# Performance work log

Measured on AMD Instinct MI355X. Metric: run time of the kernel, lower is better.

## Reference

```python
import jax, jax.numpy as jnp
import numpy as np

NH = 8          # n_heads
EPS = 1e-12     # layer_norm_eps


def _ln(x, g, b, eps=EPS):
    m = x.mean(-1, keepdims=True)
    v = jnp.var(x, axis=-1, keepdims=True)
    return (x - m) / jnp.sqrt(v + eps) * g + b


def _heads(x):
    # [B,S,H] -> [B,NH,S,H/NH]
    B, S, H = x.shape
    return x.reshape(B, S, NH, H // NH).transpose(0, 2, 1, 3)


def setup_inputs() -> dict:
    B, S, H, INNER = 32, 512, 512, 2048
    n_items = 50000
    std = 0.02
    ks = list(jax.random.split(jax.random.key(0), 20))
    inp = {}
    inp['x'] = jax.random.normal(ks[0], (B, S, H), jnp.float32)
    inp['value_input'] = jax.random.normal(ks[1], (B, S, H), jnp.float32)
    inp['beha_emb'] = jax.random.normal(ks[2], (B, S, H), jnp.float32)
    inp['pos_table'] = std * jax.random.normal(ks[3], (S, H), jnp.float32)
    names = ['q', 'k', 'v', 'pk', 'pq', 'bk', 'bq', 'd']
    for i, n in enumerate(names):
        inp['W' + n] = std * jax.random.normal(ks[4 + i], (H, H), jnp.float32)
        inp['b' + n] = jnp.zeros((H,), jnp.float32)
    inp['ln_g'] = jnp.ones((H,), jnp.float32)
    inp['ln_b'] = jnp.zeros((H,), jnp.float32)
    inp['W1'] = std * jax.random.normal(ks[12], (H, INNER), jnp.float32)
    inp['b1'] = jnp.zeros((INNER,), jnp.float32)
    inp['W2'] = std * jax.random.normal(ks[13], (INNER, H), jnp.float32)
    inp['b2'] = jnp.zeros((H,), jnp.float32)
    inp['ln2_g'] = jnp.ones((H,), jnp.float32)
    inp['ln2_b'] = jnp.zeros((H,), jnp.float32)
    inp['item_seq'] = jax.random.randint(ks[14], (B, S), 0, n_items, jnp.int32)
    return inp


def reference(x, value_input, beha_emb, pos_table, Wq, bq, Wk, bk, Wv, bv,
              Wpk, bpk, Wpq, bpq, Wbk, bbk, Wbq, bbq, Wd, bd, ln_g, ln_b,
              W1, b1, W2, b2, ln2_g, ln2_b, item_seq):
    B, S, H = x.shape
    dh = H // NH
    pos = pos_table[:S][None]  # [1,S,H] position_embedding(arange(S))

    q = _heads(x @ Wq + bq)
    k = _heads(x @ Wk + bk)
    v = _heads(value_input @ Wv + bv + value_input)  # value(value_input) + value_input
    pk = _heads(jnp.broadcast_to(pos @ Wpk + bpk, (B, S, H)))
    pq = _heads(jnp.broadcast_to(pos @ Wpq + bpq, (B, S, H)))
    bhk = _heads(beha_emb @ Wbk + bbk)
    bhq = _heads(beha_emb @ Wbq + bbq)

    # disentangled score: q.k^T + q.((beha_k+pos_k)/2)^T + ((beha_q+pos_q)/2).k^T
    scores = (jnp.einsum('bhqd,bhkd->bhqk', q, k)
              + jnp.einsum('bhqd,bhkd->bhqk', q, (bhk + pk) * 0.5)
              + jnp.einsum('bhqd,bhkd->bhqk', (bhq + pq) * 0.5, k))
    scores = scores / (dh ** 0.5)

    # causal + padding mask: (1 - mask) * -10000
    valid = item_seq > 0                              # [B,S]
    causal = jnp.tril(jnp.ones((S, S), bool))         # [S,S]
    ok = valid[:, None, None, :] & causal[None, None]
    scores = scores + jnp.where(ok, 0.0, -10000.0)

    probs = jax.nn.softmax(scores, axis=-1)
    ctx = jnp.einsum('bhqk,bhkd->bhqd', probs, v)
    ctx = ctx.transpose(0, 2, 1, 3).reshape(B, S, H)

    attn_out = _ln(ctx @ Wd + bd + x, ln_g, ln_b)

    # FeedForward (RecBole): dense1 -> gelu -> dense2 -> LN(residual)
    h = jax.nn.gelu(attn_out @ W1 + b1, approximate=False)
    h = h @ W2 + b2
    return _ln(h + attn_out, ln2_g, ln2_b)
```

## Files before the change

### kernel.cpp

```cpp
#include <hip/hip_runtime.h>
#include <math.h>


typedef unsigned short u16;
typedef __attribute__((ext_vector_type(8))) short bf16x8;
typedef __attribute__((ext_vector_type(4))) float f32x4;

#define NM 16384

__device__ __forceinline__ u16 f2b(float f) {
  union { float f; unsigned u; } x; x.f = f;
  return (u16)((x.u + 0x7fffu + ((x.u >> 16) & 1u)) >> 16);
}
__device__ __forceinline__ float b2f(u16 u) {
  union { unsigned u; float f; } x; x.u = ((unsigned)u) << 16; return x.f;
}
__device__ __forceinline__ f32x4 mfma16(bf16x8 a, bf16x8 b, f32x4 c) {
  return __builtin_amdgcn_mfma_f32_16x16x32_bf16(a, b, c, 0, 0, 0);
}
__device__ __forceinline__ void gl16(const u16* g, u16* l) {
  __builtin_amdgcn_global_load_lds(
      (const __attribute__((address_space(1))) unsigned int*)(const void*)g,
      (__attribute__((address_space(3))) unsigned int*)(void*)l, 16, 0, 0);
}
__device__ __forceinline__ bf16x8 baddv(bf16x8 a, bf16x8 b) {
  bf16x8 r;
  #pragma unroll
  for (int e = 0; e < 8; ++e) r[e] = (short)f2b(b2f((u16)a[e]) + b2f((u16)b[e]));
  return r;
}

__device__ __forceinline__ void kloop(
    const u16* __restrict__ A, const u16* __restrict__ W,
    int m0, int n0, int K, int kiters, u16* sm,
    f32x4 (&acc)[4][4])
{
  const int tid = threadIdx.x;
  const int wave = tid>>6, lane = tid&63, quad = lane>>4, l16 = lane&15;
  const int wm = wave>>1, wn = wave&1;
  const int r1 = tid>>2;
  const int ch1 = (((tid&3) ^ ((r1>>1)&3)) << 3);
  const int qsw = ((quad ^ ((l16>>1)&3)) << 3);
  const u16* pA = A + (size_t)(m0+r1)*K + ch1;
  const u16* pB = W + (size_t)(n0+r1)*K + ch1;
  u16* s0 = sm + tid*8;
  gl16(pA, s0);            gl16(pA + (size_t)64*K, s0 + 2048);
  gl16(pB, s0 + 4096);     gl16(pB + (size_t)64*K, s0 + 6144);
  if (kiters > 1) {
    u16* s1 = s0 + 8192;
    gl16(pA + 32, s1);          gl16(pA + (size_t)64*K + 32, s1 + 2048);
    gl16(pB + 32, s1 + 4096);   gl16(pB + (size_t)64*K + 32, s1 + 6144);
    asm volatile("s_waitcnt vmcnt(4)" ::: "memory");
  } else {
    asm volatile("s_waitcnt vmcnt(0)" ::: "memory");
  }
  __builtin_amdgcn_s_barrier();
  int buf = 0;
  for (int it = 0; it < kiters; ++it) {
    if (it + 2 < kiters) {
      const int kn = (it + 2)*32;
      int nb = buf - 1; if (nb < 0) nb += 3;
      u16* sn = s0 + nb*8192;
      gl16(pA + kn, sn);           gl16(pA + (size_t)64*K + kn, sn + 2048);
      gl16(pB + kn, sn + 4096);    gl16(pB + (size_t)64*K + kn, sn + 6144);
    }
    const u16* As = sm + buf*8192;
    const u16* Bs = As + 4096;
    bf16x8 af[4], bf[4];
    #pragma unroll
    for (int i = 0; i < 4; ++i)
      af[i] = *(const bf16x8*)&As[(wm*64 + i*16 + l16)*32 + qsw];
    #pragma unroll
    for (int j = 0; j < 4; ++j)
      bf[j] = *(const bf16x8*)&Bs[(wn*64 + j*16 + l16)*32 + qsw];
    __builtin_amdgcn_s_setprio(1);
    #pragma unroll
    for (int i = 0; i < 4; ++i)
      #pragma unroll
      for (int j = 0; j < 4; ++j)
        acc[i][j] = mfma16(af[i], bf[j], acc[i][j]);
    __builtin_amdgcn_s_setprio(0);
    if (it + 2 < kiters)
      asm volatile("s_waitcnt vmcnt(4)" ::: "memory");
    else
      asm volatile("s_waitcnt vmcnt(0)" ::: "memory");
    __builtin_amdgcn_s_barrier();
    buf = (buf + 1 == 3) ? 0 : buf + 1;
  }
}

__device__ __forceinline__ void kloop256(
    const u16* __restrict__ A, const u16* __restrict__ W,
    int m0, int n0, int K, int kiters, u16* sm,
    f32x4 (&acc)[8][4])
{
  const int tid = threadIdx.x;
  const int wave = tid>>6, lane = tid&63, quad = lane>>4, l16 = lane&15;
  const int wm = wave>>2, wn = wave&3;
  const int r1 = tid>>2;
  const int ch1 = (((tid&3) ^ ((r1>>1)&3)) << 3);
  const int qsw = ((quad ^ ((l16>>1)&3)) << 3);
  const u16* pA = A + (size_t)(m0+r1)*K + ch1;
  const u16* pB = W + (size_t)(n0+r1)*K + ch1;
  u16* s0 = sm + tid*8;
  gl16(pA, s0);             gl16(pA + (size_t)128*K, s0 + 4096);
  gl16(pB, s0 + 8192);      gl16(pB + (size_t)128*K, s0 + 12288);
  if (kiters > 1) {
    u16* s1 = s0 + 16384;
    gl16(pA + 32, s1);           gl16(pA + (size_t)128*K + 32, s1 + 4096);
    gl16(pB + 32, s1 + 8192);    gl16(pB + (size_t)128*K + 32, s1 + 12288);
    asm volatile("s_waitcnt vmcnt(4)" ::: "memory");
  } else {
    asm volatile("s_waitcnt vmcnt(0)" ::: "memory");
  }
  __builtin_amdgcn_s_barrier();
  int buf = 0;
  for (int it = 0; it < kiters; ++it) {
    if (it + 2 < kiters) {
      const int kn = (it + 2)*32;
      int nb = buf - 1; if (nb < 0) nb += 3;
      u16* sn = s0 + nb*16384;
      gl16(pA + kn, sn);           gl16(pA + (size_t)128*K + kn, sn + 4096);
      gl16(pB + kn, sn + 8192);    gl16(pB + (size_t)128*K + kn, sn + 12288);
    }
    const u16* As = sm + buf*16384;
    const u16* Bs = As + 8192;
    bf16x8 bf[4];
    #pragma unroll
    for (int j = 0; j < 4; ++j)
      bf[j] = *(const bf16x8*)&Bs[(wn*64 + j*16 + l16)*32 + qsw];
    #pragma unroll
    for (int ih = 0; ih < 2; ++ih) {
      bf16x8 af[4];
      #pragma unroll
      for (int ii = 0; ii < 4; ++ii)
        af[ii] = *(const bf16x8*)&As[(wm*128 + (ih*4+ii)*16 + l16)*32 + qsw];
      __builtin_amdgcn_s_setprio(1);
      #pragma unroll
      for (int ii = 0; ii < 4; ++ii)
        #pragma unroll
        for (int j = 0; j < 4; ++j)
          acc[ih*4+ii][j] = mfma16(af[ii], bf[j], acc[ih*4+ii][j]);
      __builtin_amdgcn_s_setprio(0);
    }
    if (it + 2 < kiters)
      asm volatile("s_waitcnt vmcnt(4)" ::: "memory");
    else
      asm volatile("s_waitcnt vmcnt(0)" ::: "memory");
    __builtin_amdgcn_s_barrier();
    buf = (buf + 1 == 3) ? 0 : buf + 1;
  }
}

template<int GELU>
__device__ __forceinline__ void epi256(
    f32x4 (&acc)[8][4], const float* __restrict__ bias,
    const u16* __restrict__ ex, int exmode, float scale,
    u16* __restrict__ out, int m0, int n0, int N, u16* til)
{
  const int tid = threadIdx.x;
  const int wave = tid>>6, lane = tid&63, quad = lane>>4, l16 = lane&15;
  const int wm = wave>>2, wn = wave&3;
  #pragma unroll
  for (int pass = 0; pass < 2; ++pass) {
    if (wm == pass) {
      #pragma unroll
      for (int j = 0; j < 4; ++j) {
        const int c = wn*64 + j*16 + l16;
        const float bv = bias[n0 + c];
        #pragma unroll
        for (int i = 0; i < 8; ++i)
          #pragma unroll
          for (int rr = 0; rr < 4; ++rr) {
            float v = acc[i][j][rr] + bv;
            if (GELU) v = 0.5f*v*(1.0f + erff(v*0.70710678118654752f));
            til[(i*16 + quad*4 + rr)*264 + c] = f2b(v);
          }
      }
    }
    __syncthreads();
    const int r = tid>>2, ck = tid&3;
    const int gr = m0 + pass*128 + r;
    #pragma unroll
    for (int c8 = 0; c8 < 8; ++c8) {
      const int cc = (ck + 4*c8)*8, gc = n0 + cc;
      u16 e8[8];
      *(uint4*)e8 = *(const uint4*)&til[r*264 + cc];
      if (exmode) {
        const u16* ep = &ex[(size_t)(gr & 511)*512 + gc];
        #pragma unroll
        for (int e = 0; e < 8; ++e) e8[e] = f2b((b2f(e8[e]) + b2f(ep[e]))*scale);
      } else if (scale != 1.0f) {
        #pragma unroll
        for (int e = 0; e < 8; ++e) e8[e] = f2b(b2f(e8[e])*scale);
      }
      *(uint4*)&out[(size_t)gr*N + gc] = *(uint4*)e8;
    }
    __syncthreads();
  }
}

__device__ __forceinline__ void epi_std(
    f32x4 (&acc)[4][4], const float* __restrict__ bias,
    const u16* __restrict__ ex, int exmode, float scale, int gelu,
    u16* __restrict__ out, int m0, int n0, int N, u16* til)
{
  const int tid = threadIdx.x;
  const int wave = tid>>6, lane = tid&63, quad = lane>>4, l16 = lane&15;
  const int wm = wave>>1, wn = wave&1;
  #pragma unroll
  for (int pass = 0; pass < 2; ++pass) {
    if (wm == pass) {
      #pragma unroll
      for (int j = 0; j < 4; ++j) {
        const int c = wn*64 + j*16 + l16;
        const float bv = bias[n0 + c];
        #pragma unroll
        for (int i = 0; i < 4; ++i)
          #pragma unroll
          for (int rr = 0; rr < 4; ++rr) {
            float v = acc[i][j][rr] + bv;
            if (gelu) v = 0.5f*v*(1.0f + erff(v*0.70710678118654752f));
            til[(i*16 + quad*4 + rr)*136 + c] = f2b(v);
          }
      }
    }
    __syncthreads();
    const int r = tid>>2, ck = tid&3;
    const int gr = m0 + pass*64 + r;
    #pragma unroll
    for (int kk = 0; kk < 4; ++kk) {
      const int cc = ck*32 + kk*8, gc = n0 + cc;
      u16 e8[8];
      *(uint4*)e8 = *(const uint4*)&til[r*136 + cc];
      if (exmode) {
        const u16* ep = (exmode == 1) ? &ex[(size_t)(gr & 511)*512 + gc]
                                      : &ex[(size_t)gr*512 + gc];
        #pragma unroll
        for (int e = 0; e < 8; ++e) e8[e] = f2b((b2f(e8[e]) + b2f(ep[e]))*scale);
      } else if (scale != 1.0f) {
        #pragma unroll
        for (int e = 0; e < 8; ++e) e8[e] = f2b(b2f(e8[e])*scale);
      }
      *(uint4*)&out[(size_t)gr*N + gc] = *(uint4*)e8;
    }
    __syncthreads();
  }
}

__device__ __forceinline__ void epi_vt(
    f32x4 (&acc)[4][4], const float* __restrict__ bias,
    u16* __restrict__ Vt, int m0, int n0, u16* til)
{
  const int tid = threadIdx.x;
  const int wave = tid>>6, lane = tid&63, quad = lane>>4, l16 = lane&15;
  const int wm = wave>>1, wn = wave&1;
  const int b = m0 >> 9, s0 = m0 & 511;
  #pragma unroll
  for (int pass = 0; pass < 2; ++pass) {
    if (wn == pass) {
      #pragma unroll
      for (int j = 0; j < 4; ++j) {
        const int cl = j*16 + l16;
        const float bv = bias[n0 + pass*64 + cl];
        #pragma unroll
        for (int i = 0; i < 4; ++i)
          #pragma unroll
          for (int rr = 0; rr < 4; ++rr)
            til[cl*136 + wm*64 + i*16 + quad*4 + rr] = f2b(acc[i][j][rr] + bv);
      }
    }
    __syncthreads();
    const int cl = tid>>2, ck = tid&3;
    const int gn = n0 + pass*64 + cl, h = gn>>6, d = gn&63;
    u16* orow = Vt + ((size_t)((b*8 + h)*64 + d))*512 + s0 + ck*32;
    #pragma unroll
    for (int kk = 0; kk < 4; ++kk)
      *(uint4*)&orow[kk*8] = *(const uint4*)&til[cl*136 + ck*32 + kk*8];
    __syncthreads();
  }
}

struct PJ { const u16* A; const u16* W; const float* bias; const u16* ex;
            u16* out; float scale; int exmode; int epiv; };
struct ProjArgs { PJ p[7]; };

__global__ __launch_bounds__(256, 2) void proj_kernel(ProjArgs pa, int phaseBase) {
  __shared__ __align__(16) u16 smem[24576];
  const int nbx = gridDim.x;
  const int nwg = nbx * gridDim.y;
  int lin = blockIdx.y*nbx + blockIdx.x;
  lin = (lin & 7)*(nwg >> 3) + (lin >> 3);
  const int bx = lin % nbx, by = lin / nbx;
  const PJ P = pa.p[phaseBase + (bx >> 2)];
  const int n0 = (bx & 3)*128, m0 = by*128;
  f32x4 acc[4][4] = {};
  kloop(P.A, P.W, m0, n0, 512, 16, smem, acc);
  if (P.epiv) epi_vt(acc, P.bias, P.out, m0, n0, smem);
  else        epi_std(acc, P.bias, P.ex, P.exmode, P.scale, 0, P.out, m0, n0, 512, smem);
}

__global__ __launch_bounds__(512, 1) void proj256_kernel(ProjArgs pa) {
  __shared__ __align__(16) u16 smem[49152];
  const int nbx = gridDim.x;
  const int nwg = nbx * gridDim.y;
  int lin = blockIdx.y*nbx + blockIdx.x;
  lin = (lin & 7)*(nwg >> 3) + (lin >> 3);
  const int bx = lin % nbx, by = lin / nbx;
  const PJ P = pa.p[bx >> 1];
  const int n0 = (bx & 1)*256, m0 = by*256;
  f32x4 acc[8][4] = {};
  kloop256(P.A, P.W, m0, n0, 512, 16, smem, acc);
  epi256<0>(acc, P.bias, P.ex, P.exmode, P.scale, P.out, m0, n0, 512, smem);
}

template<int GELU>
__global__ __launch_bounds__(256, 2) void gemm1_kernel(
    const u16* __restrict__ A, const u16* __restrict__ W,
    const float* __restrict__ bias, u16* __restrict__ out, int N, int K)
{
  __shared__ __align__(16) u16 smem[24576];
  const int nbx = gridDim.x;
  const int nwg = nbx * gridDim.y;
  int lin = blockIdx.y*nbx + blockIdx.x;
  lin = (lin & 7)*(nwg >> 3) + (lin >> 3);
  const int m0 = (lin / nbx)*128, n0 = (lin % nbx)*128;
  f32x4 acc[4][4] = {};
  kloop(A, W, m0, n0, K, K>>5, smem, acc);
  epi_std(acc, bias, nullptr, 0, 1.0f, GELU, out, m0, n0, N, smem);
}

template<int GELU>
__global__ __launch_bounds__(512, 1) void gemm256_kernel(
    const u16* __restrict__ A, const u16* __restrict__ W,
    const float* __restrict__ bias, u16* __restrict__ out, int N, int K)
{
  __shared__ __align__(16) u16 smem[49152];
  const int nbx = gridDim.x;
  const int nwg = nbx * gridDim.y;
  int lin = blockIdx.y*nbx + blockIdx.x;
  lin = (lin & 7)*(nwg >> 3) + (lin >> 3);
  const int m0 = (lin / nbx)*256, n0 = (lin % nbx)*256;
  f32x4 acc[8][4] = {};
  kloop256(A, W, m0, n0, K, K>>5, smem, acc);
  epi256<GELU>(acc, bias, nullptr, 0, 1.0f, out, m0, n0, N, smem);
}

__global__ __launch_bounds__(256) void cast_all_kernel(
    const float* __restrict__ x, const float* __restrict__ v,
    const float* __restrict__ be, const float* __restrict__ pos,
    u16* __restrict__ xb, u16* __restrict__ vb, u16* __restrict__ bb,
    u16* __restrict__ posb)
{
  int z = blockIdx.y;
  const float* in = (z==0) ? x : (z==1) ? v : (z==2) ? be : pos;
  u16* out = (z==0) ? xb : (z==1) ? vb : (z==2) ? bb : posb;
  int n4 = (z < 3) ? (NM*512/4) : (512*512/4);
  int i = blockIdx.x*256 + threadIdx.x;
  if (i >= n4) return;
  float4 w = ((const float4*)in)[i];
  ((ushort4*)out)[i] = make_ushort4(f2b(w.x), f2b(w.y), f2b(w.z), f2b(w.w));
}

struct PrepArgs {
  const float* w[10];
  u16* o[10];
  const float* bbq; const float* bbk;
  float* Bq2; float* Bk2;
};
__global__ __launch_bounds__(256) void wprep_all_kernel(PrepArgs a) {
  int job = blockIdx.x;
  if (job == 1024) {
    for (int i = threadIdx.x; i < 512; i += 256) {
      a.Bq2[i] = 0.5f*a.bbq[i];
      a.Bk2[i] = 0.5f*a.bbk[i];
    }
    return;
  }
  int wsel, n0, k0, K, N;
  if (job < 512)      { wsel = job>>6; int t = job&63;  n0=(t&7)*64;  k0=(t>>3)*64; K=512;  N=512; }
  else if (job < 768) { wsel = 8;      int t = job-512; n0=(t&31)*64; k0=(t>>5)*64; K=512;  N=2048; }
  else                { wsel = 9;      int t = job-768; n0=(t&7)*64;  k0=(t>>3)*64; K=2048; N=512; }
  float sc = (wsel == 5 || wsel == 6) ? 0.5f : 1.0f;
  const float* in = a.w[wsel];
  u16* out = a.o[wsel];
  __shared__ __align__(16) u16 til[64*72];
  for (int idx = threadIdx.x; idx < 4096; idx += 256) {
    int r = idx>>6, c = idx&63;
    float val = in[(size_t)(k0+r)*N + n0+c] * sc;
    if (wsel == 2 && (k0+r) == (n0+c)) val += 1.0f;
    til[r*72+c] = f2b(val);
  }
  __syncthreads();
  for (int idx = threadIdx.x; idx < 4096; idx += 256) {
    int r = idx>>6, c = idx&63;
    out[(size_t)(n0+r)*K + k0+c] = til[c*72+r];
  }
}

__global__ __launch_bounds__(512, 2) void attn_kernel(
    const u16* __restrict__ Qraw, const u16* __restrict__ Praw,
    const u16* __restrict__ Kraw, const u16* __restrict__ Mraw,
    const u16* __restrict__ Vt, const int* __restrict__ iseq,
    u16* __restrict__ ctx)
{
  const int qh = blockIdx.x, h = blockIdx.y, b = blockIdx.z;
  const int tid = threadIdx.x;
  const int wave = tid>>6, lane = tid&63, quad = lane>>4, l16 = lane&15;

  __shared__ __align__(16) u16 Ks[2][64*136];
  __shared__ __align__(16) u16 Vs[2][64*72];
  __shared__ __align__(16) u16 Ps[8][16*72];
  __shared__ float sel[512];

  const int q0 = qh*256;
  const int ntiles = 4*qh + 4;
  const u16* Kg = Kraw + (size_t)(b*512)*512 + h*64;
  const u16* Mg = Mraw + (size_t)(b*512)*512 + h*64;
  const u16* Vg = Vt + (size_t)((b*8 + h)*64)*512;

  if (tid < 512) sel[tid] = (iseq[b*512 + tid] > 0) ? 1.0f : 1e-30f;

  bf16x8 aq[2][4];
  #pragma unroll
  for (int s = 0; s < 2; ++s) {
    const size_t ro = (size_t)(b*512 + q0 + s*128 + wave*16 + l16)*512 + h*64;
    bf16x8 qf0 = *(const bf16x8*)&Qraw[ro + quad*8];
    bf16x8 qf1 = *(const bf16x8*)&Qraw[ro + 32 + quad*8];
    bf16x8 pf0 = *(const bf16x8*)&Praw[ro + quad*8];
    bf16x8 pf1 = *(const bf16x8*)&Praw[ro + 32 + quad*8];
    aq[s][0] = baddv(qf0, pf0); aq[s][1] = baddv(qf1, pf1);
    aq[s][2] = qf0;             aq[s][3] = qf1;
  }

  const int sr = tid>>3, sc8 = (tid&7)*8;
  uint4 kreg = *(const uint4*)&Kg[(size_t)sr*512 + sc8];
  uint4 mreg = *(const uint4*)&Mg[(size_t)sr*512 + sc8];
  uint4 vreg = *(const uint4*)&Vg[(size_t)sr*512 + sc8];

  f32x4 Ob[2][4] = {};
  float lrow[2][4] = {};
  u16* Pw = Ps[wave];
  int buf = 0;

  for (int kt = 0; kt < ntiles; ++kt) {
    const int k0 = kt*64;
    *(uint4*)&Ks[buf][sr*136 + sc8]      = kreg;
    *(uint4*)&Ks[buf][sr*136 + 64 + sc8] = mreg;
    *(uint4*)&Vs[buf][sr*72 + sc8]       = vreg;
    __syncthreads();
    if (kt + 1 < ntiles) {
      const int kn = k0 + 64;
      kreg = *(const uint4*)&Kg[(size_t)(kn + sr)*512 + sc8];
      mreg = *(const uint4*)&Mg[(size_t)(kn + sr)*512 + sc8];
      vreg = *(const uint4*)&Vg[(size_t)sr*512 + kn + sc8];
    }
    const bool act0 = (q0 + wave*16 + 15) >= k0;
    const bool act1 = (q0 + 128 + wave*16 + 15) >= k0;
    if (act1) {
      f32x4 sc[2][4] = {};
      #pragma unroll
      for (int ks = 0; ks < 4; ++ks) {
        bf16x8 bk[4];
        #pragma unroll
        for (int j = 0; j < 4; ++j)
          bk[j] = *(const bf16x8*)&Ks[buf][(j*16 + l16)*136 + ks*32 + quad*8];
        if (act0) {
          #pragma unroll
          for (int j = 0; j < 4; ++j) sc[0][j] = mfma16(aq[0][ks], bk[j], sc[0][j]);
        }
        #pragma unroll
        for (int j = 0; j < 4; ++j) sc[1][j] = mfma16(aq[1][ks], bk[j], sc[1][j]);
      }
      #pragma unroll
      for (int s = 0; s < 2; ++s) {
        if (s == 0 && !act0) continue;
        const int rb = q0 + s*128 + wave*16 + quad*4;
        float pj[4][4];
        #pragma unroll
        for (int j = 0; j < 4; ++j) {
          int col = k0 + j*16 + l16;
          float fs = sel[col];
          #pragma unroll
          for (int r = 0; r < 4; ++r) {
            float m2 = (col <= rb + r) ? fs : 1e-30f;
            pj[j][r] = __expf(sc[s][j][r]) * m2;
          }
        }
        #pragma unroll
        for (int r = 0; r < 4; ++r)
          lrow[s][r] += pj[0][r] + pj[1][r] + pj[2][r] + pj[3][r];
        #pragma unroll
        for (int j = 0; j < 4; ++j)
          #pragma unroll
          for (int r = 0; r < 4; ++r)
            Pw[(quad*4 + r)*72 + j*16 + l16] = f2b(pj[j][r]);
        #pragma unroll
        for (int c = 0; c < 4; ++c) {
          #pragma unroll
          for (int k2 = 0; k2 < 2; ++k2) {
            bf16x8 ap = *(const bf16x8*)&Pw[l16*72 + k2*32 + quad*8];
            bf16x8 bv = *(const bf16x8*)&Vs[buf][(c*16 + l16)*72 + k2*32 + quad*8];
            Ob[s][c] = mfma16(ap, bv, Ob[s][c]);
          }
        }
      }
    }
    buf ^= 1;
  }

  #pragma unroll
  for (int s = 0; s < 2; ++s) {
    #pragma unroll
    for (int r = 0; r < 4; ++r) {
      float l = lrow[s][r];
      #pragma unroll
      for (int d2 = 1; d2 < 16; d2 <<= 1) l += __shfl_xor(l, d2, 64);
      float inv = 1.0f / l;
      int grow = b*512 + q0 + s*128 + wave*16 + quad*4 + r;
      #pragma unroll
      for (int c = 0; c < 4; ++c)
        ctx[(size_t)grow*512 + h*64 + c*16 + l16] = f2b(Ob[s][c][r]*inv);
    }
  }
}

template<int RES>
__global__ __launch_bounds__(256) void ln_kernel(
    const u16* __restrict__ a, const void* __restrict__ resv,
    const float* __restrict__ g, const float* __restrict__ be,
    float* __restrict__ of, u16* __restrict__ ob)
{
  const int wave = threadIdx.x >> 6, lane = threadIdx.x & 63;
  const int row = blockIdx.x*4 + wave;
  const ushort4* pa = (const ushort4*)(a + (size_t)row*512);
  ushort4 a0 = pa[lane], a1 = pa[lane+64];
  float v[8] = { b2f(a0.x), b2f(a0.y), b2f(a0.z), b2f(a0.w),
                 b2f(a1.x), b2f(a1.y), b2f(a1.z), b2f(a1.w) };
  if (RES == 1) {
    const ushort4* pr = (const ushort4*)((const u16*)resv + (size_t)row*512);
    ushort4 u0 = pr[lane], u1 = pr[lane+64];
    v[0]+=b2f(u0.x); v[1]+=b2f(u0.y); v[2]+=b2f(u0.z); v[3]+=b2f(u0.w);
    v[4]+=b2f(u1.x); v[5]+=b2f(u1.y); v[6]+=b2f(u1.z); v[7]+=b2f(u1.w);
  } else {
    const float4* pr = (const float4*)((const float*)resv + (size_t)row*512);
    float4 r0 = pr[lane], r1 = pr[lane+64];
    v[0]+=r0.x; v[1]+=r0.y; v[2]+=r0.z; v[3]+=r0.w;
    v[4]+=r1.x; v[5]+=r1.y; v[6]+=r1.z; v[7]+=r1.w;
  }
  float s = 0.f, q = 0.f;
  #pragma unroll
  for (int e = 0; e < 8; ++e) { s += v[e]; q += v[e]*v[e]; }
  #pragma unroll
  for (int d = 1; d < 64; d <<= 1) { s += __shfl_xor(s, d, 64); q += __shfl_xor(q, d, 64); }
  float mean = s * (1.0f/512.0f);
  float var  = q * (1.0f/512.0f) - mean*mean;
  float rstd = rsqrtf(var + 1e-12f);
  float4 g0 = ((const float4*)g)[lane],  g1 = ((const float4*)g)[lane+64];
  float4 b0 = ((const float4*)be)[lane], b1 = ((const float4*)be)[lane+64];
  float o[8];
  o[0]=(v[0]-mean)*rstd*g0.x+b0.x; o[1]=(v[1]-mean)*rstd*g0.y+b0.y;
  o[2]=(v[2]-mean)*rstd*g0.z+b0.z; o[3]=(v[3]-mean)*rstd*g0.w+b0.w;
  o[4]=(v[4]-mean)*rstd*g1.x+b1.x; o[5]=(v[5]-mean)*rstd*g1.y+b1.y;
  o[6]=(v[6]-mean)*rstd*g1.z+b1.z; o[7]=(v[7]-mean)*rstd*g1.w+b1.w;
  if (of) {
    ((float4*)(of + (size_t)row*512))[lane]    = make_float4(o[0],o[1],o[2],o[3]);
    ((float4*)(of + (size_t)row*512))[lane+64] = make_float4(o[4],o[5],o[6],o[7]);
  }
  if (ob) {
    ((ushort4*)(ob + (size_t)row*512))[lane]    = make_ushort4(f2b(o[0]),f2b(o[1]),f2b(o[2]),f2b(o[3]));
    ((ushort4*)(ob + (size_t)row*512))[lane+64] = make_ushort4(f2b(o[4]),f2b(o[5]),f2b(o[6]),f2b(o[7]));
  }
}

extern "C" void kernel_launch(void* const* d_in, const int* in_sizes, int n_in,
                              void* d_out, int out_size, void* d_ws, size_t ws_size,
                              hipStream_t stream) {
  (void)in_sizes; (void)n_in; (void)out_size; (void)ws_size;
  const float* x    = (const float*)d_in[0];
  const float* vin  = (const float*)d_in[1];
  const float* beh  = (const float*)d_in[2];
  const float* pos  = (const float*)d_in[3];
  const float* bq   = (const float*)d_in[5];
  const float* bk   = (const float*)d_in[7];
  const float* bv   = (const float*)d_in[9];
  const float* bpk  = (const float*)d_in[11];
  const float* bpq  = (const float*)d_in[13];
  const float* bbk  = (const float*)d_in[15];
  const float* bbq  = (const float*)d_in[17];
  const float* bd   = (const float*)d_in[19];
  const float* ln_g = (const float*)d_in[20];
  const float* ln_b = (const float*)d_in[21];
  const float* b1   = (const float*)d_in[23];
  const float* b2   = (const float*)d_in[25];
  const float* ln2_g= (const float*)d_in[26];
  const float* ln2_b= (const float*)d_in[27];
  const int*   iseq = (const int*)d_in[28];
  float* out = (float*)d_out;
  char* ws = (char*)d_ws;

  size_t off = 0;
  auto nxt = [&](size_t sz) { size_t r = off; off += (sz + 255) & ~(size_t)255; return r; };
  size_t oWT[8]; for (int i = 0; i < 8; ++i) oWT[i] = nxt(512*512*2);
  size_t oW1T = nxt((size_t)512*2048*2);
  size_t oW2T = nxt((size_t)512*2048*2);
  size_t oBq2 = nxt(512*4);
  size_t oBk2 = nxt(512*4);
  size_t oPb  = nxt(512*512*2);
  size_t oPQ  = nxt(512*512*2);
  size_t oPK  = nxt(512*512*2);
  size_t oXb  = nxt((size_t)NM*512*2);
  size_t oVb  = nxt((size_t)NM*512*2);
  size_t oBb  = nxt((size_t)NM*512*2);
  size_t oQr  = nxt((size_t)NM*512*2);
  size_t oPr  = nxt((size_t)NM*512*2);
  size_t oKr  = nxt((size_t)NM*512*2);
  size_t oMr  = nxt((size_t)NM*512*2);
  size_t oVt  = nxt((size_t)NM*512*2);

  u16* WT[8]; for (int i = 0; i < 8; ++i) WT[i] = (u16*)(ws + oWT[i]);
  u16*   W1T  = (u16*)(ws + oW1T);
  u16*   W2T  = (u16*)(ws + oW2T);
  float* Bq2  = (float*)(ws + oBq2);
  float* Bk2  = (float*)(ws + oBk2);
  u16*   posb = (u16*)(ws + oPb);
  u16*   PQs  = (u16*)(ws + oPQ);
  u16*   PKs  = (u16*)(ws + oPK);
  u16*   xb   = (u16*)(ws + oXb);
  u16*   vb   = (u16*)(ws + oVb);
  u16*   bb   = (u16*)(ws + oBb);
  u16*   Qraw = (u16*)(ws + oQr);
  u16*   Praw = (u16*)(ws + oPr);
  u16*   Kraw = (u16*)(ws + oKr);
  u16*   Mraw = (u16*)(ws + oMr);
  u16*   Vtb  = (u16*)(ws + oVt);
  u16*   Cb   = (u16*)(ws + oVb);
  u16*   db   = (u16*)(ws + oPr);
  u16*   ab   = (u16*)(ws + oXb);
  u16*   h1b  = (u16*)(ws + oQr);
  u16*   f2   = (u16*)(ws + oVt);

  cast_all_kernel<<<dim3(8192, 4), 256, 0, stream>>>(x, vin, beh, pos, xb, vb, bb, posb);
  PrepArgs pr;
  const int wi[10] = {4, 6, 8, 10, 12, 14, 16, 18, 22, 24};
  for (int i = 0; i < 10; ++i) pr.w[i] = (const float*)d_in[wi[i]];
  for (int i = 0; i < 8; ++i)  pr.o[i] = WT[i];
  pr.o[8] = W1T; pr.o[9] = W2T;
  pr.bbq = bbq; pr.bbk = bbk; pr.Bq2 = Bq2; pr.Bk2 = Bk2;
  wprep_all_kernel<<<1025, 256, 0, stream>>>(pr);
  ProjArgs pj;
  pj.p[0] = { xb,   WT[0], bq,   nullptr, Qraw, 0.125f, 0, 0 };
  pj.p[1] = { xb,   WT[1], bk,   nullptr, Kraw, 1.0f,   0, 0 };
  pj.p[2] = { bb,   WT[6], Bq2,  PQs,     Praw, 0.125f, 1, 0 };
  pj.p[3] = { bb,   WT[5], Bk2,  PKs,     Mraw, 1.0f,   1, 0 };
  pj.p[4] = { vb,   WT[2], bv,   nullptr, Vtb,  1.0f,   0, 1 };
  pj.p[5] = { posb, WT[4], bpq,  nullptr, PQs,  0.5f,   0, 0 };
  pj.p[6] = { posb, WT[3], bpk,  nullptr, PKs,  0.5f,   0, 0 };
  proj_kernel<<<dim3(8, 4), 256, 0, stream>>>(pj, 5);
  proj256_kernel<<<dim3(8, 64), 512, 0, stream>>>(pj);
  proj_kernel<<<dim3(4, 128), 256, 0, stream>>>(pj, 4);
  attn_kernel<<<dim3(2, 8, 32), 512, 0, stream>>>(Qraw, Praw, Kraw, Mraw, Vtb, iseq, Cb);
  gemm1_kernel<0><<<dim3(4, 128), 256, 0, stream>>>(Cb, WT[7], bd, db, 512, 512);
  ln_kernel<0><<<4096, 256, 0, stream>>>(db, x, ln_g, ln_b, nullptr, ab);
  gemm256_kernel<1><<<dim3(8, 64), 512, 0, stream>>>(ab, W1T, b1, h1b, 2048, 512);
  gemm1_kernel<0><<<dim3(4, 128), 256, 0, stream>>>(h1b, W2T, b2, f2, 512, 2048);
  ln_kernel<1><<<4096, 256, 0, stream>>>(f2, ab, ln2_g, ln2_b, out, nullptr);
}
```

Measured before the change: 507.3 us.

## Rework 256-tile GEMM mainloop into 8-phase double-buffered K=64 pipeline; merge projections

```diff
diff --git a/kernel.cpp b/kernel.cpp
--- a/kernel.cpp
+++ b/kernel.cpp
@@ -89,9 +89,9 @@
   }
 }
 
-__device__ __forceinline__ void kloop256(
+__device__ __forceinline__ void kloop8p(
     const u16* __restrict__ A, const u16* __restrict__ W,
-    int m0, int n0, int K, int kiters, u16* sm,
+    int m0, int n0, int K, int ntiles, u16* sm,
     f32x4 (&acc)[8][4])
 {
   const int tid = threadIdx.x;
@@ -102,39 +102,40 @@
   const int qsw = ((quad ^ ((l16>>1)&3)) << 3);
   const u16* pA = A + (size_t)(m0+r1)*K + ch1;
   const u16* pB = W + (size_t)(n0+r1)*K + ch1;
-  u16* s0 = sm + tid*8;
-  gl16(pA, s0);             gl16(pA + (size_t)128*K, s0 + 4096);
-  gl16(pB, s0 + 8192);      gl16(pB + (size_t)128*K, s0 + 12288);
-  if (kiters > 1) {
-    u16* s1 = s0 + 16384;
-    gl16(pA + 32, s1);           gl16(pA + (size_t)128*K + 32, s1 + 4096);
-    gl16(pB + 32, s1 + 8192);    gl16(pB + (size_t)128*K + 32, s1 + 12288);
-    asm volatile("s_waitcnt vmcnt(4)" ::: "memory");
-  } else {
-    asm volatile("s_waitcnt vmcnt(0)" ::: "memory");
-  }
+  {
+    u16* d = sm + tid*8;
+    gl16(pA,      d);          gl16(pA + (size_t)128*K,      d + 4096);
+    gl16(pA + 32, d + 8192);   gl16(pA + (size_t)128*K + 32, d + 12288);
+    gl16(pB,      d + 16384);  gl16(pB + (size_t)128*K,      d + 20480);
+    gl16(pB + 32, d + 24576);  gl16(pB + (size_t)128*K + 32, d + 28672);
+  }
+  asm volatile("s_waitcnt vmcnt(0)" ::: "memory");
   __builtin_amdgcn_s_barrier();
-  int buf = 0;
-  for (int it = 0; it < kiters; ++it) {
-    if (it + 2 < kiters) {
-      const int kn = (it + 2)*32;
-      int nb = buf - 1; if (nb < 0) nb += 3;
-      u16* sn = s0 + nb*16384;
-      gl16(pA + kn, sn);           gl16(pA + (size_t)128*K + kn, sn + 4096);
-      gl16(pB + kn, sn + 8192);    gl16(pB + (size_t)128*K + kn, sn + 12288);
-    }
-    const u16* As = sm + buf*16384;
-    const u16* Bs = As + 8192;
+  for (int t = 0; t < ntiles; ++t) {
+    const int b = t & 1;
+    const u16* Ab = sm + b*32768;
+    const u16* Bb = Ab + 16384;
+    u16* dn = sm + (b^1)*32768 + tid*8;
     bf16x8 bf[4];
     #pragma unroll
-    for (int j = 0; j < 4; ++j)
-      bf[j] = *(const bf16x8*)&Bs[(wn*64 + j*16 + l16)*32 + qsw];
-    #pragma unroll
-    for (int ih = 0; ih < 2; ++ih) {
+    for (int p = 0; p < 4; ++p) {
+      const int kk = p >> 1, ih = p & 1;
       bf16x8 af[4];
       #pragma unroll
       for (int ii = 0; ii < 4; ++ii)
-        af[ii] = *(const bf16x8*)&As[(wm*128 + (ih*4+ii)*16 + l16)*32 + qsw];
+        af[ii] = *(const bf16x8*)&Ab[kk*8192 + (wm*128 + (ih*4+ii)*16 + l16)*32 + qsw];
+      if (ih == 0) {
+        #pragma unroll
+        for (int j = 0; j < 4; ++j)
+          bf[j] = *(const bf16x8*)&Bb[kk*8192 + (wn*64 + j*16 + l16)*32 + qsw];
+      }
+      if (t + 1 < ntiles) {
+        const int kb = (t+1)*64 + (p&1)*32;
+        const u16* src = (p < 2) ? (pA + kb) : (pB + kb);
+        u16* dst = dn + (p < 2 ? 0 : 16384) + (p&1)*8192;
+        gl16(src, dst);  gl16(src + (size_t)128*K, dst + 4096);
+      }
+      __builtin_amdgcn_s_barrier();
       __builtin_amdgcn_s_setprio(1);
       #pragma unroll
       for (int ii = 0; ii < 4; ++ii)
@@ -142,20 +143,16 @@
         for (int j = 0; j < 4; ++j)
           acc[ih*4+ii][j] = mfma16(af[ii], bf[j], acc[ih*4+ii][j]);
       __builtin_amdgcn_s_setprio(0);
-    }
-    if (it + 2 < kiters)
-      asm volatile("s_waitcnt vmcnt(4)" ::: "memory");
-    else
-      asm volatile("s_waitcnt vmcnt(0)" ::: "memory");
-    __builtin_amdgcn_s_barrier();
-    buf = (buf + 1 == 3) ? 0 : buf + 1;
+      if (p == 3)
+        asm volatile("s_waitcnt vmcnt(0)" ::: "memory");
+      __builtin_amdgcn_s_barrier();
+    }
   }
 }
 
 template<int GELU>
 __device__ __forceinline__ void epi256(
     f32x4 (&acc)[8][4], const float* __restrict__ bias,
-    const u16* __restrict__ ex, int exmode, float scale,
     u16* __restrict__ out, int m0, int n0, int N, u16* til)
 {
   const int tid = threadIdx.x;
@@ -184,17 +181,7 @@
     #pragma unroll
     for (int c8 = 0; c8 < 8; ++c8) {
       const int cc = (ck + 4*c8)*8, gc = n0 + cc;
-      u16 e8[8];
-      *(uint4*)e8 = *(const uint4*)&til[r*264 + cc];
-      if (exmode) {
-        const u16* ep = &ex[(size_t)(gr & 511)*512 + gc];
-        #pragma unroll
-        for (int e = 0; e < 8; ++e) e8[e] = f2b((b2f(e8[e]) + b2f(ep[e]))*scale);
-      } else if (scale != 1.0f) {
-        #pragma unroll
-        for (int e = 0; e < 8; ++e) e8[e] = f2b(b2f(e8[e])*scale);
-      }
-      *(uint4*)&out[(size_t)gr*N + gc] = *(uint4*)e8;
+      *(uint4*)&out[(size_t)gr*N + gc] = *(const uint4*)&til[r*264 + cc];
     }
     __syncthreads();
   }
@@ -300,20 +287,6 @@
   else        epi_std(acc, P.bias, P.ex, P.exmode, P.scale, 0, P.out, m0, n0, 512, smem);
 }
 
-__global__ __launch_bounds__(512, 1) void proj256_kernel(ProjArgs pa) {
-  __shared__ __align__(16) u16 smem[49152];
-  const int nbx = gridDim.x;
-  const int nwg = nbx * gridDim.y;
-  int lin = blockIdx.y*nbx + blockIdx.x;
-  lin = (lin & 7)*(nwg >> 3) + (lin >> 3);
-  const int bx = lin % nbx, by = lin / nbx;
-  const PJ P = pa.p[bx >> 1];
-  const int n0 = (bx & 1)*256, m0 = by*256;
-  f32x4 acc[8][4] = {};
-  kloop256(P.A, P.W, m0, n0, 512, 16, smem, acc);
-  epi256<0>(acc, P.bias, P.ex, P.exmode, P.scale, P.out, m0, n0, 512, smem);
-}
-
 template<int GELU>
 __global__ __launch_bounds__(256, 2) void gemm1_kernel(
     const u16* __restrict__ A, const u16* __restrict__ W,
@@ -331,19 +304,19 @@
 }
 
 template<int GELU>
-__global__ __launch_bounds__(512, 1) void gemm256_kernel(
+__global__ __launch_bounds__(512, 1) void gemm8p_kernel(
     const u16* __restrict__ A, const u16* __restrict__ W,
     const float* __restrict__ bias, u16* __restrict__ out, int N, int K)
 {
-  __shared__ __align__(16) u16 smem[49152];
+  __shared__ __align__(16) u16 smem[65536];
   const int nbx = gridDim.x;
   const int nwg = nbx * gridDim.y;
   int lin = blockIdx.y*nbx + blockIdx.x;
   lin = (lin & 7)*(nwg >> 3) + (lin >> 3);
   const int m0 = (lin / nbx)*256, n0 = (lin % nbx)*256;
   f32x4 acc[8][4] = {};
-  kloop256(A, W, m0, n0, K, K>>5, smem, acc);
-  epi256<GELU>(acc, bias, nullptr, 0, 1.0f, out, m0, n0, N, smem);
+  kloop8p(A, W, m0, n0, K, K>>6, smem, acc);
+  epi256<GELU>(acc, bias, out, m0, n0, N, smem);
 }
 
 __global__ __launch_bounds__(256) void cast_all_kernel(
@@ -657,12 +630,11 @@
   pj.p[5] = { posb, WT[4], bpq,  nullptr, PQs,  0.5f,   0, 0 };
   pj.p[6] = { posb, WT[3], bpk,  nullptr, PKs,  0.5f,   0, 0 };
   proj_kernel<<<dim3(8, 4), 256, 0, stream>>>(pj, 5);
-  proj256_kernel<<<dim3(8, 64), 512, 0, stream>>>(pj);
-  proj_kernel<<<dim3(4, 128), 256, 0, stream>>>(pj, 4);
+  proj_kernel<<<dim3(20, 128), 256, 0, stream>>>(pj, 0);
   attn_kernel<<<dim3(2, 8, 32), 512, 0, stream>>>(Qraw, Praw, Kraw, Mraw, Vtb, iseq, Cb);
   gemm1_kernel<0><<<dim3(4, 128), 256, 0, stream>>>(Cb, WT[7], bd, db, 512, 512);
   ln_kernel<0><<<4096, 256, 0, stream>>>(db, x, ln_g, ln_b, nullptr, ab);
-  gemm256_kernel<1><<<dim3(8, 64), 512, 0, stream>>>(ab, W1T, b1, h1b, 2048, 512);
+  gemm8p_kernel<1><<<dim3(8, 64), 512, 0, stream>>>(ab, W1T, b1, h1b, 2048, 512);
   gemm1_kernel<0><<<dim3(4, 128), 256, 0, stream>>>(h1b, W2T, b2, f2, 512, 2048);
   ln_kernel<1><<<4096, 256, 0, stream>>>(f2, ab, ln2_g, ln2_b, out, nullptr);
 }
```

Result: no change. 507.8 us (+0.1%).
